# Kernel optimization log

Measured on AMD Instinct MI355X. Metric: run time of the kernel, lower is better.

Reference implementation:

```python
import jax, jax.numpy as jnp
import numpy as np

HIDDEN = 3584
NUM_HEADS = 28
NUM_KV_HEADS = 4
HEAD_DIM = 128
ROPE_THETA = 1000000.0
B, S = 2, 2048


def setup_inputs() -> dict:
    key = jax.random.key(0)
    k1, k2, k3, k4 = jax.random.split(key, 4)
    q_size = NUM_HEADS * HEAD_DIM
    kv_size = NUM_KV_HEADS * HEAD_DIM
    return {
        "positions": jnp.arange(B * S, dtype=jnp.int32).reshape(B, S),
        "hidden_states": jax.random.normal(k1, (B, S, HIDDEN), dtype=jnp.float32),
        "w_qkv": jax.random.normal(k2, (HIDDEN, q_size + 2 * kv_size), dtype=jnp.float32) * (HIDDEN ** -0.5),
        "b_qkv": jax.random.normal(k3, (q_size + 2 * kv_size,), dtype=jnp.float32) * 0.02,
        "w_o": jax.random.normal(k4, (q_size, HIDDEN), dtype=jnp.float32) * (q_size ** -0.5),
    }


def _rope_cos_sin(positions):
    # NeoX-style rotary embedding, rotary_dim == head_dim
    half = HEAD_DIM // 2
    inv_freq = 1.0 / (ROPE_THETA ** (jnp.arange(0, half, dtype=jnp.float32) * 2.0 / HEAD_DIM))
    angles = positions.astype(jnp.float32)[..., None] * inv_freq  # [B, S, half]
    return jnp.cos(angles), jnp.sin(angles)


def _apply_rope(x, cos, sin):
    # x: [B, S, H, D]; cos/sin: [B, S, half] -> broadcast over heads
    x1, x2 = jnp.split(x, 2, axis=-1)
    c = cos[:, :, None, :]
    s = sin[:, :, None, :]
    return jnp.concatenate([x1 * c - x2 * s, x2 * c + x1 * s], axis=-1)


def reference(positions, hidden_states, w_qkv, b_qkv, w_o):
    q_size = NUM_HEADS * HEAD_DIM
    kv_size = NUM_KV_HEADS * HEAD_DIM
    scaling = HEAD_DIM ** -0.5
    groups = NUM_HEADS // NUM_KV_HEADS

    qkv = hidden_states @ w_qkv + b_qkv  # [B, S, q+2kv]
    q, k, v = jnp.split(qkv, [q_size, q_size + kv_size], axis=-1)
    q = q.reshape(B, S, NUM_HEADS, HEAD_DIM)
    k = k.reshape(B, S, NUM_KV_HEADS, HEAD_DIM)
    v = v.reshape(B, S, NUM_KV_HEADS, HEAD_DIM)

    cos, sin = _rope_cos_sin(positions)
    q = _apply_rope(q, cos, sin)
    k = _apply_rope(k, cos, sin)

    # GQA: group query heads over kv heads. q: [B, S, Hkv, G, D]
    qg = q.reshape(B, S, NUM_KV_HEADS, groups, HEAD_DIM)
    scores = jnp.einsum("bqhgd,bkhd->bhgqk", qg, k) * scaling  # [B, Hkv, G, S, S]
    causal = jnp.tril(jnp.ones((S, S), dtype=bool))
    scores = jnp.where(causal, scores, jnp.finfo(scores.dtype).min)
    probs = jax.nn.softmax(scores, axis=-1)
    o = jnp.einsum("bhgqk,bkhd->bqhgd", probs, v)  # [B, S, Hkv, G, D]
    o = o.reshape(B, S, NUM_HEADS * HEAD_DIM)
    return o @ w_o  # [B, S, HIDDEN]
```

## Files before the change

### kernel.cpp

```cpp
#include <hip/hip_runtime.h>

typedef unsigned short u16;
typedef unsigned int u32;
typedef __bf16 bf16x8 __attribute__((ext_vector_type(8)));
typedef float f32x4 __attribute__((ext_vector_type(4)));

#define NHEAD 28
#define NKVH 4
#define HD 128
#define NB 2
#define NS 2048
#define NTOK 4096
#define HIDDEN_DIM 3584
#define QKVW 4608
#define QSZ 3584
#define KOFF 3584
#define VOFF 4096
#define VSLAB (NTOK * 512)
#define NJOBS 896
#define ATTN_BLOCKS 512
#define QSCALE_L2E 0.12751744f

__device__ __forceinline__ float bf2f(u16 u) {
  u32 x = ((u32)u) << 16; float f; __builtin_memcpy(&f, &x, 4); return f;
}
__device__ __forceinline__ u16 f2bf(float f) {
  u32 x; __builtin_memcpy(&x, &f, 4);
  x += 0x7FFFu + ((x >> 16) & 1u);
  return (u16)(x >> 16);
}
__device__ __forceinline__ u32 pack2bf(float a, float b) {
  __bf16 lo = (__bf16)a, hi = (__bf16)b;
  u16 ul, uh;
  __builtin_memcpy(&ul, &lo, 2); __builtin_memcpy(&uh, &hi, 2);
  return (u32)ul | ((u32)uh << 16);
}
__device__ __forceinline__ void async16(const void* g, void* lds) {
  __builtin_amdgcn_global_load_lds((const __attribute__((address_space(1))) void*)g,
                                   (__attribute__((address_space(3))) void*)lds,
                                   16, 0, 0);
}

#define SB __builtin_amdgcn_sched_barrier(0)
#define BAR do { SB; __builtin_amdgcn_s_barrier(); SB; } while (0)

__global__ void cast_f32_bf16(const float* __restrict__ in, u16* __restrict__ out) {
  int i = (blockIdx.x * 256 + threadIdx.x) * 4;
  float4 v = *(const float4*)(in + i);
  u32 p0 = (u32)f2bf(v.x) | ((u32)f2bf(v.y) << 16);
  u32 p1 = (u32)f2bf(v.z) | ((u32)f2bf(v.w) << 16);
  uint2 r; r.x = p0; r.y = p1;
  *(uint2*)(out + i) = r;
}

__global__ void transpose_cast(const float* __restrict__ in, u16* __restrict__ out,
                               int R, int C) {
  __shared__ float tile[32][33];
  int tx = threadIdx.x & 31, ty = threadIdx.x >> 5;
  int c0 = blockIdx.x * 32, r0 = blockIdx.y * 32;
#pragma unroll
  for (int i = 0; i < 32; i += 8)
    tile[ty + i][tx] = in[(size_t)(r0 + ty + i) * C + c0 + tx];
  __syncthreads();
#pragma unroll
  for (int i = 0; i < 32; i += 8)
    out[(size_t)(c0 + ty + i) * R + r0 + tx] = f2bf(tile[tx][ty + i]);
}

__global__ void rope_table(const int* __restrict__ positions,
                           float* __restrict__ cs, float* __restrict__ sn,
                           int* __restrict__ ctr) {
  if (blockIdx.x == 0 && threadIdx.x == 0) *ctr = 0;
  int idx = blockIdx.x * 256 + threadIdx.x;
  int t = idx >> 6, i = idx & 63;
  float p = (float)positions[t];
  float inv = expf(-(float)i * (13.815510557964274f / 64.f));
  float a = p * inv;
  cs[idx] = cosf(a);
  sn[idx] = sinf(a);
}

__global__ void rope_kernel(u16* __restrict__ qkv, const float* __restrict__ cs,
                            const float* __restrict__ sn) {
  const int gtid = blockIdx.x * 256 + threadIdx.x;
  const int hr = gtid >> 4;
  const int sub = gtid & 15;
  const int t = hr >> 5, hh = hr & 31;
  const size_t base = (size_t)t * QKVW +
                      (hh < NHEAD ? hh * HD : KOFF + (hh - NHEAD) * HD);
  const int d0 = sub * 4;
  uint2 xa = *(const uint2*)(qkv + base + d0);
  uint2 xb = *(const uint2*)(qkv + base + 64 + d0);
  float4 c = *(const float4*)(cs + t * 64 + d0);
  float4 s = *(const float4*)(sn + t * 64 + d0);
  float x1[4], x2[4];
  x1[0] = bf2f((u16)xa.x); x1[1] = bf2f((u16)(xa.x >> 16));
  x1[2] = bf2f((u16)xa.y); x1[3] = bf2f((u16)(xa.y >> 16));
  x2[0] = bf2f((u16)xb.x); x2[1] = bf2f((u16)(xb.x >> 16));
  x2[2] = bf2f((u16)xb.y); x2[3] = bf2f((u16)(xb.y >> 16));
  const float cc[4] = {c.x, c.y, c.z, c.w};
  const float ss[4] = {s.x, s.y, s.z, s.w};
  const float sc = (hh < NHEAD) ? QSCALE_L2E : 1.0f;
  float y1[4], y2[4];
#pragma unroll
  for (int i = 0; i < 4; ++i) {
    y1[i] = (x1[i] * cc[i] - x2[i] * ss[i]) * sc;
    y2[i] = (x2[i] * cc[i] + x1[i] * ss[i]) * sc;
  }
  uint2 ra, rb;
  ra.x = pack2bf(y1[0], y1[1]); ra.y = pack2bf(y1[2], y1[3]);
  rb.x = pack2bf(y2[0], y2[1]); rb.y = pack2bf(y2[2], y2[3]);
  *(uint2*)(qkv + base + d0) = ra;
  *(uint2*)(qkv + base + 64 + d0) = rb;
}

template <int MODE>
__global__ __launch_bounds__(512, 2) void gemm256(
    const u16* __restrict__ A, const u16* __restrict__ Bt,
    const float* __restrict__ bias, u16* __restrict__ outb,
    float* __restrict__ outf, int M, int Next, int Kst, int ldc, int NT) {
  __shared__ __align__(16) u16 Al[2][256 * 64];
  __shared__ __align__(16) u16 Bl[2][256 * 64];
  const int tid = threadIdx.x;
  const int l = tid & 63, w = tid >> 6;
  const int g = l >> 4, r = l & 15;
  const int wm = w >> 2, wn = w & 3;
  const int nbx = Next >> 8;
  const int cpx = (int)gridDim.x >> 3;
  const int bid = ((int)blockIdx.x & 7) * cpx + ((int)blockIdx.x >> 3);
  int bx, by, kbase;
  float* outp = outf;
  if (MODE == 2) {
    const int tps = nbx * (M >> 8);
    const int ks = bid / tps, rem = bid % tps;
    by = rem / nbx; bx = rem % nbx;
    kbase = ks * (NT << 6);
    outp = outf + (size_t)ks * M * Next;
  } else {
    bx = bid % nbx; by = bid / nbx; kbase = 0;
  }
  const int row0 = by * 256, col0 = bx * 256;

  f32x4 acc[8][4] = {};
  bf16x8 af[4][2];
  bf16x8 bfr[2][2][2];

  auto stageU = [&](const u16* mb, int base0, char* ldsMat, int h, int t) {
#pragma unroll
    for (int q = 0; q < 2; ++q) {
      const int idx = q * 512 + tid;
      const int rho = h * 128 + (idx >> 3);
      const int sl = (idx & 7) ^ (rho & 7);
      async16(mb + (size_t)(base0 + rho) * Kst + kbase + t * 64 + sl * 8,
              ldsMat + (size_t)(t & 1) * 32768 + h * 16384 + idx * 16);
    }
  };

#define READ_A(s, rh)                                                           \
  _Pragma("unroll") for (int fr = 0; fr < 4; ++fr) {                            \
    const int row_ = (rh) * 128 + wm * 64 + fr * 16 + r;                        \
    _Pragma("unroll") for (int kk = 0; kk < 2; ++kk) {                          \
      const int sl_ = (kk * 4 + g) ^ (row_ & 7);                                \
      af[fr][kk] = *(const bf16x8*)((const char*)Al + (s) * 32768 +             \
                                    row_ * 128 + sl_ * 16);                     \
    }                                                                           \
  }
#define READ_B(s, ch)                                                           \
  _Pragma("unroll") for (int fc = 0; fc < 2; ++fc) {                            \
    const int col_ = (ch) * 128 + wn * 32 + fc * 16 + r;                        \
    _Pragma("unroll") for (int kk = 0; kk < 2; ++kk) {                          \
      const int sl_ = (kk * 4 + g) ^ (col_ & 7);                                \
      bfr[ch][fc][kk] = *(const bf16x8*)((const char*)Bl + (s) * 32768 +        \
                                         col_ * 128 + sl_ * 16);                \
    }                                                                           \
  }
#define MFMA_Q(rh, ch)                                                          \
  __builtin_amdgcn_s_setprio(1);                                                \
  _Pragma("unroll") for (int fr = 0; fr < 4; ++fr)                              \
  _Pragma("unroll") for (int fc = 0; fc < 2; ++fc)                              \
  _Pragma("unroll") for (int kk = 0; kk < 2; ++kk)                              \
    acc[(rh) * 4 + fr][(ch) * 2 + fc] = __builtin_amdgcn_mfma_f32_16x16x32_bf16( \
        af[fr][kk], bfr[ch][fc][kk], acc[(rh) * 4 + fr][(ch) * 2 + fc], 0, 0, 0);\
  __builtin_amdgcn_s_setprio(0);

  stageU(A, row0, (char*)Al, 0, 0); stageU(A, row0, (char*)Al, 1, 0);
  stageU(Bt, col0, (char*)Bl, 0, 0); stageU(Bt, col0, (char*)Bl, 1, 0);
  stageU(A, row0, (char*)Al, 0, 1); stageU(Bt, col0, (char*)Bl, 0, 1);
  SB; asm volatile("s_waitcnt vmcnt(4)" ::: "memory");
  BAR;

  for (int t = 0; t < NT; ++t) {
    const int s = t & 1;
    READ_A(s, 0); READ_B(s, 0);
    if (t + 1 < NT) stageU(A, row0, (char*)Al, 1, t + 1);
    BAR; MFMA_Q(0, 0); BAR;
    READ_B(s, 1);
    if (t + 1 < NT) stageU(Bt, col0, (char*)Bl, 1, t + 1);
    BAR; MFMA_Q(0, 1); BAR;
    READ_A(s, 1);
    if (t + 2 < NT) stageU(A, row0, (char*)Al, 0, t + 2);
    BAR; MFMA_Q(1, 0); BAR;
    if (t + 2 < NT) stageU(Bt, col0, (char*)Bl, 0, t + 2);
    BAR; MFMA_Q(1, 1);
    if (t < NT - 2)        { SB; asm volatile("s_waitcnt vmcnt(4)" ::: "memory"); }
    else if (t == NT - 2)  { SB; asm volatile("s_waitcnt vmcnt(0)" ::: "memory"); }
    BAR;
  }
  SB; asm volatile("s_waitcnt vmcnt(0)" ::: "memory");

#pragma unroll
  for (int m = 0; m < 8; ++m) {
    const int row = row0 + (m >> 2) * 128 + wm * 64 + (m & 3) * 16 + g * 4;
#pragma unroll
    for (int n = 0; n < 4; ++n) {
      const int col = col0 + (n >> 1) * 128 + wn * 32 + (n & 1) * 16 + r;
      const float bb = (MODE == 0) ? bias[col] : 0.f;
#pragma unroll
      for (int j = 0; j < 4; ++j) {
        float v = acc[m][n][j] + bb;
        if (MODE == 0) outb[(size_t)(row + j) * ldc + col] = f2bf(v);
        else           outp[(size_t)(row + j) * ldc + col] = v;
      }
    }
  }
}

__global__ void v_reduce(const float* __restrict__ slabs, const float* __restrict__ bias,
                         u16* __restrict__ vtg) {
  __shared__ float tile[32][33];
  const int tx = threadIdx.x & 31, ty = threadIdx.x >> 5;
  const int c0 = blockIdx.x * 32;
  const int r0 = blockIdx.y * 32;
#pragma unroll
  for (int i = 0; i < 32; i += 8) {
    const size_t idx = (size_t)(r0 + ty + i) * 512 + c0 + tx;
    float s = slabs[idx] + slabs[idx + VSLAB] + slabs[idx + 2 * VSLAB] +
              slabs[idx + 3 * VSLAB];
    tile[ty + i][tx] = s + bias[VOFF + c0 + tx];
  }
  __syncthreads();
#pragma unroll
  for (int i = 0; i < 32; i += 8) {
    const int col = c0 + ty + i;
    const int row = r0 + tx;
    vtg[((size_t)((((row >> 11) * NKVH) + (col >> 7)) * HD + (col & 127))) * NS +
        (row & 2047)] = f2bf(tile[tx][ty + i]);
  }
}

__global__ __launch_bounds__(512) void attn_kernel(const u16* __restrict__ qkv,
                                                   const u16* __restrict__ vtg,
                                                   u16* __restrict__ Oh,
                                                   int* __restrict__ ctr) {
  __shared__ __align__(16) u16 Ks[2][64 * 128];
  __shared__ __align__(16) u16 Vt[2][128 * 64];
  __shared__ int s_job;
  const int tid = threadIdx.x, l = tid & 63, w = tid >> 6;
  const int g = l >> 4, r = l & 15;
  const int srcA = r + ((l & 16) << 1);
  const int srcB = srcA + 16;
  const bool hi = (l & 32) != 0;

  for (;;) {
    if (tid == 0) s_job = atomicAdd(ctr, 1);
    __syncthreads();
    const int jid = s_job;
    if (jid >= NJOBS) return;
    const int qtr = jid / 56;
    const int qt = 15 - qtr;
    const int bh = jid - qtr * 56;
    const int h = bh % NHEAD, b = bh / NHEAD;
    const int kvh = h / 7;
    const int q0 = qt * 128;

    const int qrow = q0 + w * 16 + r;
    const size_t qbase = (size_t)(b * NS + qrow) * QKVW + h * HD;
    bf16x8 qf[4];
#pragma unroll
    for (int ks = 0; ks < 4; ++ks)
      qf[ks] = *(const bf16x8*)(qkv + qbase + ks * 32 + g * 8);

    const u16* kb0 = qkv + (size_t)(b * NS) * QKVW + KOFF + kvh * HD;
    const u16* vb0 = vtg + (size_t)((b * NKVH + kvh) * HD) * NS;

    const u16* kap[2];
    const u16* vap[2];
#pragma unroll
    for (int i = 0; i < 2; ++i) {
      const int li = (w * 2 + i) * 64 + l;
      const int rr = li >> 4, c = li & 15;
      kap[i] = kb0 + (size_t)rr * QKVW + ((c ^ (rr & 7)) << 3);
      const int d = li >> 3, c2 = li & 7;
      vap[i] = vb0 + (size_t)d * NS + ((c2 ^ (d & 7)) << 3);
    }

    f32x4 oacc[8] = {};
    float mrun = -1e30f, lsum = 0.f;

    const int nkv = 2 * qt + 2;

    auto stageK = [&](u16* kdst) {
#pragma unroll
      for (int i = 0; i < 2; ++i) {
        async16(kap[i], (char*)kdst + (w * 2 + i) * 1024);
        kap[i] += 64 * QKVW;
      }
    };
    auto stageV = [&](u16* vdst) {
#pragma unroll
      for (int i = 0; i < 2; ++i) {
        async16(vap[i], (char*)vdst + (w * 2 + i) * 1024);
        vap[i] += 64;
      }
    };

    stageK(Ks[0]); stageV(Vt[0]);
    int cur = 0;

    for (int kvt = 0; kvt < nkv; ++kvt) {
      const int kv0 = kvt * 64;
      asm volatile("s_waitcnt vmcnt(0)" ::: "memory");
      __builtin_amdgcn_s_barrier();
      __builtin_amdgcn_sched_barrier(0);

      const bool haveNext = (kvt + 1 < nkv);
      if (haveNext) { stageK(Ks[cur ^ 1]); stageV(Vt[cur ^ 1]); }

      const bool active = kv0 <= q0 + w * 16 + 15;

      if (active) {
        f32x4 sacc[4] = {};
        const char* ksB = (const char*)Ks[cur];
        __builtin_amdgcn_s_setprio(1);
#pragma unroll
        for (int n = 0; n < 4; ++n) {
          const int key = n * 16 + r;
          const int sw = (key & 7) << 4;
#pragma unroll
          for (int ks = 0; ks < 4; ++ks) {
            bf16x8 kf = *(const bf16x8*)(ksB + key * 256 + ((ks * 64 + g * 16) ^ sw));
            sacc[n] = __builtin_amdgcn_mfma_f32_16x16x32_bf16(kf, qf[ks], sacc[n], 0, 0, 0);
          }
        }
        __builtin_amdgcn_s_setprio(0);
        if (kv0 + 63 > q0 + w * 16) {
#pragma unroll
          for (int n = 0; n < 4; ++n) {
            const int key_g = kv0 + n * 16 + g * 4;
#pragma unroll
            for (int j = 0; j < 4; ++j)
              if (key_g + j > qrow) sacc[n][j] = -1e30f;
          }
        }
        float mx = fmaxf(fmaxf(sacc[0][0], sacc[0][1]), fmaxf(sacc[0][2], sacc[0][3]));
#pragma unroll
        for (int n = 1; n < 4; ++n)
          mx = fmaxf(mx, fmaxf(fmaxf(sacc[n][0], sacc[n][1]), fmaxf(sacc[n][2], sacc[n][3])));
        if (!__all(mx <= mrun + 8.0f)) {
          mx = fmaxf(mx, __shfl_xor(mx, 16, 64));
          mx = fmaxf(mx, __shfl_xor(mx, 32, 64));
          const float mnew = fmaxf(mrun, mx);
          const float scale = __builtin_amdgcn_exp2f(mrun - mnew);
          mrun = mnew;
          lsum *= scale;
#pragma unroll
          for (int dt = 0; dt < 8; ++dt) oacc[dt] *= scale;
        }
#pragma unroll
        for (int n = 0; n < 4; ++n)
#pragma unroll
          for (int j = 0; j < 4; ++j) {
            float p = __builtin_amdgcn_exp2f(sacc[n][j] - mrun);
            sacc[n][j] = p;
            lsum += p;
          }

        u32 pk[4][2];
#pragma unroll
        for (int n = 0; n < 4; ++n) {
          pk[n][0] = pack2bf(sacc[n][0], sacc[n][1]);
          pk[n][1] = pack2bf(sacc[n][2], sacc[n][3]);
        }
        union { u32 wrd[4]; bf16x8 v; } pf[2];
#pragma unroll
        for (int ks2 = 0; ks2 < 2; ++ks2) {
          const int n0 = 2 * ks2, n1 = 2 * ks2 + 1;
#pragma unroll
          for (int hh2 = 0; hh2 < 2; ++hh2) {
            u32 a0 = (u32)__shfl((int)pk[n0][hh2], srcA, 64);
            u32 a1 = (u32)__shfl((int)pk[n1][hh2], srcA, 64);
            pf[ks2].wrd[hh2] = hi ? a1 : a0;
            u32 b0 = (u32)__shfl((int)pk[n0][hh2], srcB, 64);
            u32 b1 = (u32)__shfl((int)pk[n1][hh2], srcB, 64);
            pf[ks2].wrd[2 + hh2] = hi ? b1 : b0;
          }
        }

        const char* vtB = (const char*)Vt[cur];
        __builtin_amdgcn_s_setprio(1);
#pragma unroll
        for (int ks2 = 0; ks2 < 2; ++ks2) {
#pragma unroll
          for (int dt = 0; dt < 8; ++dt) {
            const int d = dt * 16 + r;
            bf16x8 vf = *(const bf16x8*)(vtB + d * 128 +
                                         ((ks2 * 64 + g * 16) ^ ((d & 7) << 4)));
            oacc[dt] = __builtin_amdgcn_mfma_f32_16x16x32_bf16(vf, pf[ks2].v, oacc[dt], 0, 0, 0);
          }
        }
        __builtin_amdgcn_s_setprio(0);
      }
      cur ^= 1;
    }

    float lr = lsum;
    lr += __shfl_xor(lr, 16, 64);
    lr += __shfl_xor(lr, 32, 64);
    const float inv = 1.f / lr;
    const size_t obase = (size_t)(b * NS + qrow) * QSZ + h * HD;
#pragma unroll
    for (int dt = 0; dt < 8; ++dt) {
      uint2 r2;
      r2.x = pack2bf(oacc[dt][0] * inv, oacc[dt][1] * inv);
      r2.y = pack2bf(oacc[dt][2] * inv, oacc[dt][3] * inv);
      *(uint2*)(Oh + obase + dt * 16 + 4 * g) = r2;
    }
  }
}

extern "C" void kernel_launch(void* const* d_in, const int* in_sizes, int n_in,
                              void* d_out, int out_size, void* d_ws, size_t ws_size,
                              hipStream_t stream) {
  const int* positions = (const int*)d_in[0];
  const float* hidden = (const float*)d_in[1];
  const float* w_qkv = (const float*)d_in[2];
  const float* b_qkv = (const float*)d_in[3];
  const float* w_o = (const float*)d_in[4];
  float* out = (float*)d_out;

  char* ws = (char*)d_ws;
  const size_t XB_OFF = 0;
  const size_t WQT_OFF = 29360128;
  const size_t QKV_OFF = WQT_OFF + 33030144;
  const size_t CS_OFF = QKV_OFF + 37748736;
  const size_t SN_OFF = CS_OFF + 1048576;
  const size_t CTR_OFF = SN_OFF + 1048576;
  const size_t WS_NEED = CTR_OFF + 64;
  if (ws_size < WS_NEED) return;

  u16* Xb = (u16*)(ws + XB_OFF);
  u16* WoT = (u16*)(ws + XB_OFF);
  u16* WqT = (u16*)(ws + WQT_OFF);
  u16* Oh = (u16*)(ws + WQT_OFF);
  u16* qkvb = (u16*)(ws + QKV_OFF);
  float* cs = (float*)(ws + CS_OFF);
  float* sn = (float*)(ws + SN_OFF);
  int* ctr = (int*)(ws + CTR_OFF);
  u16* vtg = (u16*)d_out;
  float* vslabs = (float*)((char*)d_out + 4194304);

  cast_f32_bf16<<<14336, 256, 0, stream>>>(hidden, Xb);
  transpose_cast<<<dim3(QKVW / 32, HIDDEN_DIM / 32), 256, 0, stream>>>(w_qkv, WqT, HIDDEN_DIM, QKVW);
  rope_table<<<(NTOK * 64) / 256, 256, 0, stream>>>(positions, cs, sn, ctr);

  gemm256<0><<<256, 512, 0, stream>>>(
      Xb, WqT, b_qkv, qkvb, nullptr, NTOK, 4096, HIDDEN_DIM, QKVW, HIDDEN_DIM / 64);

  gemm256<2><<<128, 512, 0, stream>>>(
      Xb, WqT + (size_t)VOFF * HIDDEN_DIM, nullptr, nullptr, vslabs,
      NTOK, 512, HIDDEN_DIM, 512, HIDDEN_DIM / 64 / 4);

  v_reduce<<<dim3(512 / 32, NTOK / 32), 256, 0, stream>>>(vslabs, b_qkv, vtg);

  rope_kernel<<<(NTOK * 32 * 16) / 256, 256, 0, stream>>>(qkvb, cs, sn);

  transpose_cast<<<dim3(HIDDEN_DIM / 32, QSZ / 32), 256, 0, stream>>>(w_o, WoT, QSZ, HIDDEN_DIM);

  attn_kernel<<<ATTN_BLOCKS, 512, 0, stream>>>(qkvb, vtg, Oh, ctr);

  gemm256<1><<<(HIDDEN_DIM / 256) * (NTOK / 256), 512, 0, stream>>>(
      Oh, WoT, nullptr, nullptr, out, NTOK, HIDDEN_DIM, QSZ, HIDDEN_DIM, QSZ / 64);
}
```

Before: 434.0 us.

## Merge QK and split-K V projection GEMMs into one heterogeneous launch

Combines the QK projection GEMM (256 tiles, 56 k-steps) and the split-K V projection GEMM (128 tiles, 14 k-steps) into a single 384-block kernel. Every third block is a V split-K tile, so the short V work is spread among the long QK tiles. This removes one launch and lets the V tiles fill idle CUs alongside the QK tiles. The output GEMM is also specialised with compile-time strides. The catch is load imbalance, since the V blocks finish much sooner than the QK blocks.

```diff
diff --git a/kernel.cpp b/kernel.cpp
--- a/kernel.cpp
+++ b/kernel.cpp
@@ -114,47 +114,11 @@
   *(uint2*)(qkv + base + 64 + d0) = rb;
 }
 
-template <int MODE>
-__global__ __launch_bounds__(512, 2) void gemm256(
-    const u16* __restrict__ A, const u16* __restrict__ Bt,
-    const float* __restrict__ bias, u16* __restrict__ outb,
-    float* __restrict__ outf, int M, int Next, int Kst, int ldc, int NT) {
-  __shared__ __align__(16) u16 Al[2][256 * 64];
-  __shared__ __align__(16) u16 Bl[2][256 * 64];
-  const int tid = threadIdx.x;
-  const int l = tid & 63, w = tid >> 6;
-  const int g = l >> 4, r = l & 15;
+#define GEMM_DECLS                                                              \
+  const int tid = threadIdx.x;                                                  \
+  const int l = tid & 63, w = tid >> 6;                                         \
+  const int g = l >> 4, r = l & 15;                                             \
   const int wm = w >> 2, wn = w & 3;
-  const int nbx = Next >> 8;
-  const int cpx = (int)gridDim.x >> 3;
-  const int bid = ((int)blockIdx.x & 7) * cpx + ((int)blockIdx.x >> 3);
-  int bx, by, kbase;
-  float* outp = outf;
-  if (MODE == 2) {
-    const int tps = nbx * (M >> 8);
-    const int ks = bid / tps, rem = bid % tps;
-    by = rem / nbx; bx = rem % nbx;
-    kbase = ks * (NT << 6);
-    outp = outf + (size_t)ks * M * Next;
-  } else {
-    bx = bid % nbx; by = bid / nbx; kbase = 0;
-  }
-  const int row0 = by * 256, col0 = bx * 256;
-
-  f32x4 acc[8][4] = {};
-  bf16x8 af[4][2];
-  bf16x8 bfr[2][2][2];
-
-  auto stageU = [&](const u16* mb, int base0, char* ldsMat, int h, int t) {
-#pragma unroll
-    for (int q = 0; q < 2; ++q) {
-      const int idx = q * 512 + tid;
-      const int rho = h * 128 + (idx >> 3);
-      const int sl = (idx & 7) ^ (rho & 7);
-      async16(mb + (size_t)(base0 + rho) * Kst + kbase + t * 64 + sl * 8,
-              ldsMat + (size_t)(t & 1) * 32768 + h * 16384 + idx * 16);
-    }
-  };
 
 #define READ_A(s, rh)                                                           \
   _Pragma("unroll") for (int fr = 0; fr < 4; ++fr) {                            \
@@ -183,30 +147,134 @@
         af[fr][kk], bfr[ch][fc][kk], acc[(rh) * 4 + fr][(ch) * 2 + fc], 0, 0, 0);\
   __builtin_amdgcn_s_setprio(0);
 
-  stageU(A, row0, (char*)Al, 0, 0); stageU(A, row0, (char*)Al, 1, 0);
-  stageU(Bt, col0, (char*)Bl, 0, 0); stageU(Bt, col0, (char*)Bl, 1, 0);
-  stageU(A, row0, (char*)Al, 0, 1); stageU(Bt, col0, (char*)Bl, 0, 1);
-  SB; asm volatile("s_waitcnt vmcnt(4)" ::: "memory");
-  BAR;
-
-  for (int t = 0; t < NT; ++t) {
-    const int s = t & 1;
-    READ_A(s, 0); READ_B(s, 0);
-    if (t + 1 < NT) stageU(A, row0, (char*)Al, 1, t + 1);
-    BAR; MFMA_Q(0, 0); BAR;
-    READ_B(s, 1);
-    if (t + 1 < NT) stageU(Bt, col0, (char*)Bl, 1, t + 1);
-    BAR; MFMA_Q(0, 1); BAR;
-    READ_A(s, 1);
-    if (t + 2 < NT) stageU(A, row0, (char*)Al, 0, t + 2);
-    BAR; MFMA_Q(1, 0); BAR;
-    if (t + 2 < NT) stageU(Bt, col0, (char*)Bl, 0, t + 2);
-    BAR; MFMA_Q(1, 1);
-    if (t < NT - 2)        { SB; asm volatile("s_waitcnt vmcnt(4)" ::: "memory"); }
-    else if (t == NT - 2)  { SB; asm volatile("s_waitcnt vmcnt(0)" ::: "memory"); }
-    BAR;
-  }
+#define GEMM_MAINLOOP                                                           \
+  stageU(A, row0, (char*)Al, 0, 0); stageU(A, row0, (char*)Al, 1, 0);           \
+  stageU(Bt, col0, (char*)Bl, 0, 0); stageU(Bt, col0, (char*)Bl, 1, 0);         \
+  stageU(A, row0, (char*)Al, 0, 1); stageU(Bt, col0, (char*)Bl, 0, 1);          \
+  SB; asm volatile("s_waitcnt vmcnt(4)" ::: "memory");                          \
+  BAR;                                                                          \
+  for (int t = 0; t < NT; ++t) {                                                \
+    const int s = t & 1;                                                        \
+    READ_A(s, 0); READ_B(s, 0);                                                 \
+    if (t + 1 < NT) stageU(A, row0, (char*)Al, 1, t + 1);                       \
+    BAR; MFMA_Q(0, 0); BAR;                                                     \
+    READ_B(s, 1);                                                               \
+    if (t + 1 < NT) stageU(Bt, col0, (char*)Bl, 1, t + 1);                      \
+    BAR; MFMA_Q(0, 1); BAR;                                                     \
+    READ_A(s, 1);                                                               \
+    if (t + 2 < NT) stageU(A, row0, (char*)Al, 0, t + 2);                       \
+    BAR; MFMA_Q(1, 0); BAR;                                                     \
+    if (t + 2 < NT) stageU(Bt, col0, (char*)Bl, 0, t + 2);                      \
+    BAR; MFMA_Q(1, 1);                                                          \
+    if (t < NT - 2)        { SB; asm volatile("s_waitcnt vmcnt(4)" ::: "memory"); } \
+    else if (t == NT - 2)  { SB; asm volatile("s_waitcnt vmcnt(0)" ::: "memory"); } \
+    BAR;                                                                        \
+  }                                                                             \
   SB; asm volatile("s_waitcnt vmcnt(0)" ::: "memory");
+
+__global__ __launch_bounds__(512, 2) void gemm_qkv(
+    const u16* __restrict__ A, const u16* __restrict__ Bt0,
+    const float* __restrict__ bias, u16* __restrict__ outb,
+    float* __restrict__ slabs) {
+  __shared__ __align__(16) u16 Al[2][256 * 64];
+  __shared__ __align__(16) u16 Bl[2][256 * 64];
+  GEMM_DECLS
+  const int cpx = (int)gridDim.x >> 3;
+  const int bid = ((int)blockIdx.x & 7) * cpx + ((int)blockIdx.x >> 3);
+  const bool isV = (bid % 3) == 2;
+  int bx, by, kbase, NT;
+  const u16* Bt;
+  float* outp = slabs;
+  if (isV) {
+    const int vi = bid / 3;
+    const int ks = vi >> 5, rem = vi & 31;
+    by = rem >> 1; bx = rem & 1;
+    kbase = ks * 896; NT = 14;
+    Bt = Bt0 + (size_t)VOFF * HIDDEN_DIM;
+    outp = slabs + (size_t)ks * VSLAB;
+  } else {
+    const int qi = (bid / 3) * 2 + (bid % 3);
+    bx = qi & 15; by = qi >> 4;
+    kbase = 0; NT = 56;
+    Bt = Bt0;
+  }
+  const int row0 = by * 256, col0 = bx * 256;
+
+  f32x4 acc[8][4] = {};
+  bf16x8 af[4][2];
+  bf16x8 bfr[2][2][2];
+
+  auto stageU = [&](const u16* mb, int base0, char* ldsMat, int h, int t) {
+#pragma unroll
+    for (int q = 0; q < 2; ++q) {
+      const int idx = q * 512 + tid;
+      const int rho = h * 128 + (idx >> 3);
+      const int sl = (idx & 7) ^ (rho & 7);
+      async16(mb + (size_t)(base0 + rho) * HIDDEN_DIM + kbase + t * 64 + sl * 8,
+              ldsMat + (size_t)(t & 1) * 32768 + h * 16384 + idx * 16);
+    }
+  };
+
+  GEMM_MAINLOOP
+
+  if (isV) {
+#pragma unroll
+    for (int m = 0; m < 8; ++m) {
+      const int row = row0 + (m >> 2) * 128 + wm * 64 + (m & 3) * 16 + g * 4;
+#pragma unroll
+      for (int n = 0; n < 4; ++n) {
+        const int col = col0 + (n >> 1) * 128 + wn * 32 + (n & 1) * 16 + r;
+#pragma unroll
+        for (int j = 0; j < 4; ++j)
+          outp[(size_t)(row + j) * 512 + col] = acc[m][n][j];
+      }
+    }
+  } else {
+#pragma unroll
+    for (int m = 0; m < 8; ++m) {
+      const int row = row0 + (m >> 2) * 128 + wm * 64 + (m & 3) * 16 + g * 4;
+#pragma unroll
+      for (int n = 0; n < 4; ++n) {
+        const int col = col0 + (n >> 1) * 128 + wn * 32 + (n & 1) * 16 + r;
+        const float bb = bias[col];
+#pragma unroll
+        for (int j = 0; j < 4; ++j)
+          outb[(size_t)(row + j) * QKVW + col] = f2bf(acc[m][n][j] + bb);
+      }
+    }
+  }
+}
+
+__global__ __launch_bounds__(512, 2) void gemm_out(
+    const u16* __restrict__ A, const u16* __restrict__ Bt,
+    float* __restrict__ outf) {
+  __shared__ __align__(16) u16 Al[2][256 * 64];
+  __shared__ __align__(16) u16 Bl[2][256 * 64];
+  GEMM_DECLS
+  const int cpx = (int)gridDim.x >> 3;
+  const int bid = ((int)blockIdx.x & 7) * cpx + ((int)blockIdx.x >> 3);
+  const int nbx = HIDDEN_DIM >> 8;
+  const int bx = bid % nbx, by = bid / nbx;
+  const int row0 = by * 256, col0 = bx * 256;
+  const int NT = QSZ / 64;
+  const int kbase = 0;
+
+  f32x4 acc[8][4] = {};
+  bf16x8 af[4][2];
+  bf16x8 bfr[2][2][2];
+
+  auto stageU = [&](const u16* mb, int base0, char* ldsMat, int h, int t) {
+#pragma unroll
+    for (int q = 0; q < 2; ++q) {
+      const int idx = q * 512 + tid;
+      const int rho = h * 128 + (idx >> 3);
+      const int sl = (idx & 7) ^ (rho & 7);
+      async16(mb + (size_t)(base0 + rho) * QSZ + kbase + t * 64 + sl * 8,
+              ldsMat + (size_t)(t & 1) * 32768 + h * 16384 + idx * 16);
+    }
+  };
+
+  GEMM_MAINLOOP
 
 #pragma unroll
   for (int m = 0; m < 8; ++m) {
@@ -214,13 +282,9 @@
 #pragma unroll
     for (int n = 0; n < 4; ++n) {
       const int col = col0 + (n >> 1) * 128 + wn * 32 + (n & 1) * 16 + r;
-      const float bb = (MODE == 0) ? bias[col] : 0.f;
-#pragma unroll
-      for (int j = 0; j < 4; ++j) {
-        float v = acc[m][n][j] + bb;
-        if (MODE == 0) outb[(size_t)(row + j) * ldc + col] = f2bf(v);
-        else           outp[(size_t)(row + j) * ldc + col] = v;
-      }
+#pragma unroll
+      for (int j = 0; j < 4; ++j)
+        outf[(size_t)(row + j) * HIDDEN_DIM + col] = acc[m][n][j];
     }
   }
 }
@@ -463,12 +527,7 @@
   transpose_cast<<<dim3(QKVW / 32, HIDDEN_DIM / 32), 256, 0, stream>>>(w_qkv, WqT, HIDDEN_DIM, QKVW);
   rope_table<<<(NTOK * 64) / 256, 256, 0, stream>>>(positions, cs, sn, ctr);
 
-  gemm256<0><<<256, 512, 0, stream>>>(
-      Xb, WqT, b_qkv, qkvb, nullptr, NTOK, 4096, HIDDEN_DIM, QKVW, HIDDEN_DIM / 64);
-
-  gemm256<2><<<128, 512, 0, stream>>>(
-      Xb, WqT + (size_t)VOFF * HIDDEN_DIM, nullptr, nullptr, vslabs,
-      NTOK, 512, HIDDEN_DIM, 512, HIDDEN_DIM / 64 / 4);
+  gemm_qkv<<<384, 512, 0, stream>>>(Xb, WqT, b_qkv, qkvb, vslabs);
 
   v_reduce<<<dim3(512 / 32, NTOK / 32), 256, 0, stream>>>(vslabs, b_qkv, vtg);
 
@@ -478,6 +537,5 @@
 
   attn_kernel<<<ATTN_BLOCKS, 512, 0, stream>>>(qkvb, vtg, Oh, ctr);
 
-  gemm256<1><<<(HIDDEN_DIM / 256) * (NTOK / 256), 512, 0, stream>>>(
-      Oh, WoT, nullptr, nullptr, out, NTOK, HIDDEN_DIM, QSZ, HIDDEN_DIM, QSZ / 64);
-}
+  gemm_out<<<(HIDDEN_DIM / 256) * (NTOK / 256), 512, 0, stream>>>(Oh, WoT, out);
+}
```

Result: slower. 480.8 us (+10.8%).
